# Optimization experiments

Hardware: AMD Instinct MI355X
Metric: run time of the kernel (lower is better)

The kernel has to match this reference:

```python
import jax, jax.numpy as jnp
import numpy as np

B, S, D, H = 8, 1024, 1024, 16
HD = D // H  # head dim = 64


def setup_inputs() -> dict:
    key = jax.random.key(0)
    ks = jax.random.split(key, 8)
    return {
        "hidden_states": jax.random.normal(ks[0], (B, S, D), dtype=jnp.float32),
        "attention_mask": jnp.zeros((B, 1, 1, S), dtype=jnp.float32),
        "Wq": jax.random.normal(ks[1], (D, D), dtype=jnp.float32) * (1.0 / np.sqrt(D)),
        "bq": jax.random.normal(ks[2], (D,), dtype=jnp.float32) * 0.02,
        "Wk": jax.random.normal(ks[3], (D, D), dtype=jnp.float32) * (1.0 / np.sqrt(D)),
        "bk": jax.random.normal(ks[4], (D,), dtype=jnp.float32) * 0.02,
        "Wv": jax.random.normal(ks[5], (D, D), dtype=jnp.float32) * (1.0 / np.sqrt(D)),
        "bv": jax.random.normal(ks[6], (D,), dtype=jnp.float32) * 0.02,
    }


def _split_heads(x):
    # [B,S,D] -> [B,H,S,HD]
    return x.reshape(B, S, H, HD).transpose(0, 2, 1, 3)


def reference(hidden_states, attention_mask, Wq, bq, Wk, bk, Wv, bv):
    q = _split_heads(hidden_states @ Wq + bq)
    k = _split_heads(hidden_states @ Wk + bk)
    v = _split_heads(hidden_states @ Wv + bv)
    # [B,H,S,S]
    scores = jnp.einsum("bhqd,bhkd->bhqk", q, k) / jnp.sqrt(jnp.float32(HD))
    scores = scores + attention_mask
    probs = jax.nn.softmax(scores, axis=-1)  # dropout p=0.0 (eval)
    ctx = jnp.einsum("bhqk,bhkd->bhqd", probs, v)
    # [B,H,S,HD] -> [B,S,D]
    return ctx.transpose(0, 2, 1, 3).reshape(B, S, D)
```

## Files before the change

kernel.cpp:

```cpp
#include <hip/hip_runtime.h>
#include <stdint.h>

#define BB 8
#define SS 1024
#define DD 1024
#define HH 16
#define HDIM 64

typedef __bf16 bf16x8 __attribute__((ext_vector_type(8)));
typedef float f32x4 __attribute__((ext_vector_type(4)));

__device__ __forceinline__ unsigned short f2bf(float f) {
    union { float f; unsigned u; } v; v.f = f;
    unsigned r = v.u + 0x7fff + ((v.u >> 16) & 1);
    return (unsigned short)(r >> 16);
}

__device__ __forceinline__ float exp2fast(float x) {
#if __has_builtin(__builtin_amdgcn_exp2f)
    return __builtin_amdgcn_exp2f(x);
#else
    return __expf(x * 0.69314718f);
#endif
}

__device__ __forceinline__ void async16(void* lds, const void* g) {
    __builtin_amdgcn_global_load_lds(
        (const __attribute__((address_space(1))) unsigned int*)g,
        (__attribute__((address_space(3))) unsigned int*)lds, 16, 0, 0);
}

__global__ __launch_bounds__(256) void convert_x(const float* __restrict__ x,
                                                 unsigned short* __restrict__ xb, int n) {
    int i = (blockIdx.x * 256 + threadIdx.x) * 4;
    if (i < n) {
        float4 f = *reinterpret_cast<const float4*>(x + i);
        ushort4 o;
        o.x = f2bf(f.x); o.y = f2bf(f.y); o.z = f2bf(f.z); o.w = f2bf(f.w);
        *reinterpret_cast<ushort4*>(xb + i) = o;
    }
}

__global__ __launch_bounds__(256) void transpose_w(const float* __restrict__ w0,
                                                   const float* __restrict__ w1,
                                                   const float* __restrict__ w2,
                                                   unsigned short* __restrict__ t0,
                                                   unsigned short* __restrict__ t1,
                                                   unsigned short* __restrict__ t2) {
    const float* w = (blockIdx.z == 0) ? w0 : (blockIdx.z == 1) ? w1 : w2;
    unsigned short* wt = (blockIdx.z == 0) ? t0 : (blockIdx.z == 1) ? t1 : t2;
    __shared__ unsigned short tile[64][65];
    int k0 = blockIdx.x * 64, n0 = blockIdx.y * 64;
    #pragma unroll
    for (int i = 0; i < 16; ++i) {
        int idx = threadIdx.x + i * 256;
        int r = idx >> 6, c = idx & 63;
        tile[r][c] = f2bf(w[(k0 + r) * DD + n0 + c]);
    }
    __syncthreads();
    #pragma unroll
    for (int i = 0; i < 16; ++i) {
        int idx = threadIdx.x + i * 256;
        int r = idx >> 6, c = idx & 63;
        wt[(n0 + r) * DD + k0 + c] = tile[c][r];
    }
}

__global__ __launch_bounds__(256) void gemm_qkv(
    const unsigned short* __restrict__ xb,
    const unsigned short* __restrict__ wt0, const unsigned short* __restrict__ wt1,
    const unsigned short* __restrict__ wt2,
    const float* __restrict__ b0, const float* __restrict__ b1, const float* __restrict__ b2,
    unsigned short* __restrict__ qo, unsigned short* __restrict__ ko,
    unsigned short* __restrict__ vto)
{
    const unsigned short* wt; const float* bias; unsigned short* out;
    if (blockIdx.z == 0)      { wt = wt0; bias = b0; out = qo; }
    else if (blockIdx.z == 1) { wt = wt1; bias = b1; out = ko; }
    else                      { wt = wt2; bias = b2; out = vto; }

    __shared__ unsigned short As[2][128 * 32];
    __shared__ unsigned short Bs[2][128 * 32];

    int m0 = blockIdx.x * 128, n0 = blockIdx.y * 128;
    int tid = threadIdx.x;
    int wave = tid >> 6, lane = tid & 63, lq = lane >> 4, lm = lane & 15;
    int wr = wave >> 1, wc = wave & 1;

    f32x4 acc[4][4] = {};

    int row0 = tid >> 2, s = tid & 3;
    int c0 = (s - (row0 >> 1)) & 3;
    const unsigned short* ga0 = xb + (m0 + row0) * DD + c0 * 8;
    const unsigned short* ga1 = ga0 + 64 * DD;
    const unsigned short* gb0 = wt + (n0 + row0) * DD + c0 * 8;
    const unsigned short* gb1 = gb0 + 64 * DD;

    int slot = ((lq + (lm >> 1)) & 3) * 8;

    async16(&As[0][tid * 8], ga0);  async16(&As[0][(tid + 256) * 8], ga1);
    async16(&Bs[0][tid * 8], gb0);  async16(&Bs[0][(tid + 256) * 8], gb1);
    ga0 += 32; ga1 += 32; gb0 += 32; gb1 += 32;

    for (int t = 0; t < 32; ++t) {
        int p = t & 1;
        __syncthreads();
        if (t < 31) {
            async16(&As[p ^ 1][tid * 8], ga0);  async16(&As[p ^ 1][(tid + 256) * 8], ga1);
            async16(&Bs[p ^ 1][tid * 8], gb0);  async16(&Bs[p ^ 1][(tid + 256) * 8], gb1);
            ga0 += 32; ga1 += 32; gb0 += 32; gb1 += 32;
        }
        bf16x8 a[4], b[4];
        #pragma unroll
        for (int i = 0; i < 4; ++i)
            a[i] = *reinterpret_cast<const bf16x8*>(&As[p][(wr * 64 + i * 16 + lm) * 32 + slot]);
        #pragma unroll
        for (int j = 0; j < 4; ++j)
            b[j] = *reinterpret_cast<const bf16x8*>(&Bs[p][(wc * 64 + j * 16 + lm) * 32 + slot]);
        #pragma unroll
        for (int i = 0; i < 4; ++i)
            #pragma unroll
            for (int j = 0; j < 4; ++j)
                acc[i][j] = __builtin_amdgcn_mfma_f32_16x16x32_bf16(a[i], b[j], acc[i][j], 0, 0, 0);
    }

    if (blockIdx.z == 2) {
        #pragma unroll
        for (int j = 0; j < 4; ++j) {
            int col = n0 + wc * 64 + j * 16 + lm;
            float bsv = bias[col];
            int h = col >> 6, hd = col & 63;
            #pragma unroll
            for (int i = 0; i < 4; ++i) {
                int m = m0 + wr * 64 + i * 16 + lq * 4;
                int b_ = m >> 10, sr = m & 1023;
                ushort4 pk;
                pk.x = f2bf(acc[i][j][0] + bsv);
                pk.y = f2bf(acc[i][j][1] + bsv);
                pk.z = f2bf(acc[i][j][2] + bsv);
                pk.w = f2bf(acc[i][j][3] + bsv);
                *reinterpret_cast<ushort4*>(out + (((b_ * HH + h) * HDIM + hd) << 10) + sr) = pk;
            }
        }
    } else {
        #pragma unroll
        for (int j = 0; j < 4; ++j) {
            int col = n0 + wc * 64 + j * 16 + lm;
            float bsv = bias[col];
            int h = col >> 6, hd = col & 63;
            #pragma unroll
            for (int i = 0; i < 4; ++i) {
                #pragma unroll
                for (int r = 0; r < 4; ++r) {
                    int m = m0 + wr * 64 + i * 16 + lq * 4 + r;
                    int b_ = m >> 10, sr = m & 1023;
                    out[(((b_ * HH + h) << 10) + sr) * HDIM + hd] = f2bf(acc[i][j][r] + bsv);
                }
            }
        }
    }
}

__global__ __launch_bounds__(256) void attention(
    const unsigned short* __restrict__ q,
    const unsigned short* __restrict__ k,
    const unsigned short* __restrict__ vt,
    const float* __restrict__ mask,
    float* __restrict__ out)
{
    __shared__ unsigned short Ks[2][64 * 64];
    __shared__ unsigned short Vs[2][64 * 64];
    __shared__ unsigned short Ps[4][16 * 72];
    __shared__ float msk[SS];

    int blk = blockIdx.x;
    int xcd = blk & 7, j = blk >> 3;
    int bh = (xcd << 4) + (j >> 4);
    int qt = j & 15;
    int b = bh >> 4, h = bh & 15;

    int tid = threadIdx.x;
    int wave = tid >> 6, lane = tid & 63, lq = lane >> 4, lm = lane & 15;

    const unsigned short* qp = q + (size_t)bh * SS * HDIM;
    const unsigned short* kp = k + (size_t)bh * SS * HDIM;
    const unsigned short* vp = vt + (size_t)bh * HDIM * SS;

    for (int i = tid; i < SS; i += 256) msk[i] = mask[b * SS + i] * 1.44269504f;

    int qrow = qt * 64 + wave * 16 + lm;
    bf16x8 qa0 = *reinterpret_cast<const bf16x8*>(qp + qrow * HDIM + lq * 8);
    bf16x8 qa1 = *reinterpret_cast<const bf16x8*>(qp + qrow * HDIM + 32 + lq * 8);

    float lsum = 0.f;
    f32x4 o[4] = {};

    int row0 = tid >> 3, sg = tid & 7;
    int cg = (sg - row0) & 7;
    const unsigned short* gk = kp + row0 * 64 + cg * 8;
    const unsigned short* gv = vp + row0 * SS + cg * 8;

    int sl0 = ((lq + lm) & 7) * 8;
    int sl1 = ((lq + lm + 4) & 7) * 8;

    async16(&Ks[0][tid * 8], gk);  async16(&Ks[0][(tid + 256) * 8], gk + 32 * 64);
    async16(&Vs[0][tid * 8], gv);  async16(&Vs[0][(tid + 256) * 8], gv + 32 * SS);
    gk += 64 * 64; gv += 64;

    unsigned short* Pw = Ps[wave];

    for (int t = 0; t < 16; ++t) {
        int p = t & 1;
        __syncthreads();
        if (t < 15) {
            async16(&Ks[p ^ 1][tid * 8], gk);  async16(&Ks[p ^ 1][(tid + 256) * 8], gk + 32 * 64);
            async16(&Vs[p ^ 1][tid * 8], gv);  async16(&Vs[p ^ 1][(tid + 256) * 8], gv + 32 * SS);
            gk += 64 * 64; gv += 64;
        }
        int kb0 = t * 64;

        f32x4 c[4];
        #pragma unroll
        for (int nb = 0; nb < 4; ++nb) {
            bf16x8 kf0 = *reinterpret_cast<const bf16x8*>(&Ks[p][(nb * 16 + lm) * 64 + sl0]);
            bf16x8 kf1 = *reinterpret_cast<const bf16x8*>(&Ks[p][(nb * 16 + lm) * 64 + sl1]);
            f32x4 z = {};
            z = __builtin_amdgcn_mfma_f32_16x16x32_bf16(kf0, qa0, z, 0, 0, 0);
            z = __builtin_amdgcn_mfma_f32_16x16x32_bf16(kf1, qa1, z, 0, 0, 0);
            c[nb] = z;
        }

        #pragma unroll
        for (int nb = 0; nb < 4; ++nb) {
            float4 mk = *reinterpret_cast<const float4*>(&msk[kb0 + nb * 16 + lq * 4]);
            unsigned u[4];
            #pragma unroll
            for (int r = 0; r < 4; ++r) {
                float e = exp2fast(fmaf(c[nb][r], 0.18033688f,
                                        reinterpret_cast<const float*>(&mk)[r]));
                union { float f; unsigned v; } cv; cv.f = e;
                u[r] = cv.v;
                union { unsigned v; float f; } tr; tr.v = cv.v & 0xffff0000u;
                lsum += tr.f;
            }
            uint2 pk;
            pk.x = __builtin_amdgcn_perm(u[1], u[0], 0x07060302u);
            pk.y = __builtin_amdgcn_perm(u[3], u[2], 0x07060302u);
            *reinterpret_cast<uint2*>(&Pw[lm * 72 + nb * 16 + lq * 4]) = pk;
        }

        #pragma unroll
        for (int ks = 0; ks < 2; ++ks) {
            bf16x8 pa = *reinterpret_cast<const bf16x8*>(&Pw[lm * 72 + ks * 32 + lq * 8]);
            int slv = (ks == 0) ? sl0 : sl1;
            #pragma unroll
            for (int nb2 = 0; nb2 < 4; ++nb2) {
                bf16x8 vf = *reinterpret_cast<const bf16x8*>(&Vs[p][(nb2 * 16 + lm) * 64 + slv]);
                o[nb2] = __builtin_amdgcn_mfma_f32_16x16x32_bf16(pa, vf, o[nb2], 0, 0, 0);
            }
        }
    }

    lsum += __shfl_xor(lsum, 16, 64);
    lsum += __shfl_xor(lsum, 32, 64);
    float linv[4];
    #pragma unroll
    for (int r = 0; r < 4; ++r)
        linv[r] = 1.0f / __shfl(lsum, lq * 4 + r, 64);

    #pragma unroll
    for (int nb2 = 0; nb2 < 4; ++nb2) {
        #pragma unroll
        for (int r = 0; r < 4; ++r) {
            int sr = qt * 64 + wave * 16 + lq * 4 + r;
            out[((size_t)(b * SS + sr)) * DD + h * HDIM + nb2 * 16 + lm] = o[nb2][r] * linv[r];
        }
    }
}

extern "C" void kernel_launch(void* const* d_in, const int* in_sizes, int n_in,
                              void* d_out, int out_size, void* d_ws, size_t ws_size,
                              hipStream_t stream) {
    const float* hs   = (const float*)d_in[0];
    const float* mask = (const float*)d_in[1];
    const float* Wq   = (const float*)d_in[2];
    const float* bq   = (const float*)d_in[3];
    const float* Wk   = (const float*)d_in[4];
    const float* bk   = (const float*)d_in[5];
    const float* Wv   = (const float*)d_in[6];
    const float* bv   = (const float*)d_in[7];
    float* out = (float*)d_out;

    char* ws = (char*)d_ws;
    unsigned short* Xb  = (unsigned short*)(ws);
    unsigned short* WT0 = (unsigned short*)(ws + 16777216);
    unsigned short* WT1 = (unsigned short*)(ws + 18874368);
    unsigned short* WT2 = (unsigned short*)(ws + 20971520);
    unsigned short* qw  = (unsigned short*)(ws + 23068672);
    unsigned short* kw  = (unsigned short*)(ws + 39845888);
    unsigned short* vtw = (unsigned short*)(ws + 56623104);

    convert_x<<<8192, 256, 0, stream>>>(hs, Xb, BB * SS * DD);
    transpose_w<<<dim3(16, 16, 3), 256, 0, stream>>>(Wq, Wk, Wv, WT0, WT1, WT2);
    gemm_qkv<<<dim3(64, 8, 3), 256, 0, stream>>>(Xb, WT0, WT1, WT2,
                                                 bq, bk, bv, qw, kw, vtw);
    attention<<<2048, 256, 0, stream>>>(qw, kw, vtw, mask, out);
}
```

Measured before the change: 249.3 us.

## Fuse prep kernels, remap GEMM blocks per XCD, stream A from registers, interleave attention

Merges the activation conversion and weight transpose into one launch. The QKV GEMM now uses a 1D grid that groups tiles sharing a weight strip onto the same XCD, and loads the A operand straight from global memory into double-buffered registers instead of LDS. The GEMM epilogue switches to a cheaper round-half-up bf16 pack. In attention, the mask is read from global memory instead of being staged in LDS. The QK^T, softmax and PV steps are split into halves and interleaved so MFMA work can overlap exp work, and the P buffer uses a swizzled 64-wide layout. These changes trade the round-to-nearest-even rounding for a slightly different rounding and add register pressure in the GEMM.

Result: slower. 280.8 us (+12.6%).

```diff
diff --git a/kernel.cpp b/kernel.cpp
--- a/kernel.cpp
+++ b/kernel.cpp
@@ -14,6 +14,11 @@
     union { float f; unsigned u; } v; v.f = f;
     unsigned r = v.u + 0x7fff + ((v.u >> 16) & 1);
     return (unsigned short)(r >> 16);
+}
+
+__device__ __forceinline__ unsigned pk2bf(float f0, float f1) {
+    union { float f; unsigned u; } a, b; a.f = f0; b.f = f1;
+    return __builtin_amdgcn_perm(b.u + 0x8000u, a.u + 0x8000u, 0x07060302u);
 }
 
 __device__ __forceinline__ float exp2fast(float x) {
@@ -30,38 +35,39 @@
         (__attribute__((address_space(3))) unsigned int*)lds, 16, 0, 0);
 }
 
-__global__ __launch_bounds__(256) void convert_x(const float* __restrict__ x,
-                                                 unsigned short* __restrict__ xb, int n) {
-    int i = (blockIdx.x * 256 + threadIdx.x) * 4;
-    if (i < n) {
+__global__ __launch_bounds__(256) void prep(
+    const float* __restrict__ x, unsigned short* __restrict__ xb,
+    const float* __restrict__ w0, const float* __restrict__ w1,
+    const float* __restrict__ w2,
+    unsigned short* __restrict__ t0, unsigned short* __restrict__ t1,
+    unsigned short* __restrict__ t2)
+{
+    __shared__ unsigned short tile[64][65];
+    int bid = blockIdx.x;
+    if (bid < 8192) {
+        int i = (bid * 256 + threadIdx.x) * 4;
         float4 f = *reinterpret_cast<const float4*>(x + i);
         ushort4 o;
         o.x = f2bf(f.x); o.y = f2bf(f.y); o.z = f2bf(f.z); o.w = f2bf(f.w);
         *reinterpret_cast<ushort4*>(xb + i) = o;
-    }
-}
-
-__global__ __launch_bounds__(256) void transpose_w(const float* __restrict__ w0,
-                                                   const float* __restrict__ w1,
-                                                   const float* __restrict__ w2,
-                                                   unsigned short* __restrict__ t0,
-                                                   unsigned short* __restrict__ t1,
-                                                   unsigned short* __restrict__ t2) {
-    const float* w = (blockIdx.z == 0) ? w0 : (blockIdx.z == 1) ? w1 : w2;
-    unsigned short* wt = (blockIdx.z == 0) ? t0 : (blockIdx.z == 1) ? t1 : t2;
-    __shared__ unsigned short tile[64][65];
-    int k0 = blockIdx.x * 64, n0 = blockIdx.y * 64;
+        return;
+    }
+    int idx = bid - 8192;
+    int z = idx >> 8, rem = idx & 255;
+    const float* w = (z == 0) ? w0 : (z == 1) ? w1 : w2;
+    unsigned short* wt = (z == 0) ? t0 : (z == 1) ? t1 : t2;
+    int k0 = (rem & 15) * 64, n0 = (rem >> 4) * 64;
     #pragma unroll
     for (int i = 0; i < 16; ++i) {
-        int idx = threadIdx.x + i * 256;
-        int r = idx >> 6, c = idx & 63;
+        int id = threadIdx.x + i * 256;
+        int r = id >> 6, c = id & 63;
         tile[r][c] = f2bf(w[(k0 + r) * DD + n0 + c]);
     }
     __syncthreads();
     #pragma unroll
     for (int i = 0; i < 16; ++i) {
-        int idx = threadIdx.x + i * 256;
-        int r = idx >> 6, c = idx & 63;
+        int id = threadIdx.x + i * 256;
+        int r = id >> 6, c = id & 63;
         wt[(n0 + r) * DD + k0 + c] = tile[c][r];
     }
 }
@@ -74,46 +80,55 @@
     unsigned short* __restrict__ qo, unsigned short* __restrict__ ko,
     unsigned short* __restrict__ vto)
 {
+    int bid = blockIdx.x;
+    int xcd = bid & 7, g = bid >> 3;
+    int strip = xcd * 3 + (g % 3);
+    int mt = g / 3;
+    int nt = strip & 7, z = strip >> 3;
+
     const unsigned short* wt; const float* bias; unsigned short* out;
-    if (blockIdx.z == 0)      { wt = wt0; bias = b0; out = qo; }
-    else if (blockIdx.z == 1) { wt = wt1; bias = b1; out = ko; }
-    else                      { wt = wt2; bias = b2; out = vto; }
-
-    __shared__ unsigned short As[2][128 * 32];
+    if (z == 0)      { wt = wt0; bias = b0; out = qo; }
+    else if (z == 1) { wt = wt1; bias = b1; out = ko; }
+    else             { wt = wt2; bias = b2; out = vto; }
+
     __shared__ unsigned short Bs[2][128 * 32];
 
-    int m0 = blockIdx.x * 128, n0 = blockIdx.y * 128;
+    int m0 = mt * 128, n0 = nt * 128;
     int tid = threadIdx.x;
     int wave = tid >> 6, lane = tid & 63, lq = lane >> 4, lm = lane & 15;
     int wr = wave >> 1, wc = wave & 1;
 
     f32x4 acc[4][4] = {};
 
-    int row0 = tid >> 2, s = tid & 3;
-    int c0 = (s - (row0 >> 1)) & 3;
-    const unsigned short* ga0 = xb + (m0 + row0) * DD + c0 * 8;
-    const unsigned short* ga1 = ga0 + 64 * DD;
+    int row0 = tid >> 2, s4 = tid & 3;
+    int c0 = (s4 - (row0 >> 1)) & 3;
     const unsigned short* gb0 = wt + (n0 + row0) * DD + c0 * 8;
     const unsigned short* gb1 = gb0 + 64 * DD;
 
+    const unsigned short* aBase = xb + (m0 + wr * 64 + lm) * DD + lq * 8;
+
     int slot = ((lq + (lm >> 1)) & 3) * 8;
 
-    async16(&As[0][tid * 8], ga0);  async16(&As[0][(tid + 256) * 8], ga1);
-    async16(&Bs[0][tid * 8], gb0);  async16(&Bs[0][(tid + 256) * 8], gb1);
-    ga0 += 32; ga1 += 32; gb0 += 32; gb1 += 32;
-
+    bf16x8 a[2][4];
+
+    async16(&Bs[0][tid * 8], gb0);
+    async16(&Bs[0][(tid + 256) * 8], gb1);
+    #pragma unroll
+    for (int i = 0; i < 4; ++i)
+        a[0][i] = *reinterpret_cast<const bf16x8*>(aBase + i * 16 * DD);
+
+    #pragma unroll
     for (int t = 0; t < 32; ++t) {
         int p = t & 1;
         __syncthreads();
         if (t < 31) {
-            async16(&As[p ^ 1][tid * 8], ga0);  async16(&As[p ^ 1][(tid + 256) * 8], ga1);
-            async16(&Bs[p ^ 1][tid * 8], gb0);  async16(&Bs[p ^ 1][(tid + 256) * 8], gb1);
-            ga0 += 32; ga1 += 32; gb0 += 32; gb1 += 32;
-        }
-        bf16x8 a[4], b[4];
-        #pragma unroll
-        for (int i = 0; i < 4; ++i)
-            a[i] = *reinterpret_cast<const bf16x8*>(&As[p][(wr * 64 + i * 16 + lm) * 32 + slot]);
+            async16(&Bs[p ^ 1][tid * 8], gb0 + (t + 1) * 32);
+            async16(&Bs[p ^ 1][(tid + 256) * 8], gb1 + (t + 1) * 32);
+            #pragma unroll
+            for (int i = 0; i < 4; ++i)
+                a[p ^ 1][i] = *reinterpret_cast<const bf16x8*>(aBase + i * 16 * DD + (t + 1) * 32);
+        }
+        bf16x8 b[4];
         #pragma unroll
         for (int j = 0; j < 4; ++j)
             b[j] = *reinterpret_cast<const bf16x8*>(&Bs[p][(wc * 64 + j * 16 + lm) * 32 + slot]);
@@ -121,10 +136,10 @@
         for (int i = 0; i < 4; ++i)
             #pragma unroll
             for (int j = 0; j < 4; ++j)
-                acc[i][j] = __builtin_amdgcn_mfma_f32_16x16x32_bf16(a[i], b[j], acc[i][j], 0, 0, 0);
-    }
-
-    if (blockIdx.z == 2) {
+                acc[i][j] = __builtin_amdgcn_mfma_f32_16x16x32_bf16(a[p][i], b[j], acc[i][j], 0, 0, 0);
+    }
+
+    if (z == 2) {
         #pragma unroll
         for (int j = 0; j < 4; ++j) {
             int col = n0 + wc * 64 + j * 16 + lm;
@@ -134,12 +149,10 @@
             for (int i = 0; i < 4; ++i) {
                 int m = m0 + wr * 64 + i * 16 + lq * 4;
                 int b_ = m >> 10, sr = m & 1023;
-                ushort4 pk;
-                pk.x = f2bf(acc[i][j][0] + bsv);
-                pk.y = f2bf(acc[i][j][1] + bsv);
-                pk.z = f2bf(acc[i][j][2] + bsv);
-                pk.w = f2bf(acc[i][j][3] + bsv);
-                *reinterpret_cast<ushort4*>(out + (((b_ * HH + h) * HDIM + hd) << 10) + sr) = pk;
+                uint2 pk;
+                pk.x = pk2bf(acc[i][j][0] + bsv, acc[i][j][1] + bsv);
+                pk.y = pk2bf(acc[i][j][2] + bsv, acc[i][j][3] + bsv);
+                *reinterpret_cast<uint2*>(out + (((b_ * HH + h) * HDIM + hd) << 10) + sr) = pk;
             }
         }
     } else {
@@ -154,7 +167,9 @@
                 for (int r = 0; r < 4; ++r) {
                     int m = m0 + wr * 64 + i * 16 + lq * 4 + r;
                     int b_ = m >> 10, sr = m & 1023;
-                    out[(((b_ * HH + h) << 10) + sr) * HDIM + hd] = f2bf(acc[i][j][r] + bsv);
+                    union { float f; unsigned u; } cv; cv.f = acc[i][j][r] + bsv;
+                    out[(((b_ * HH + h) << 10) + sr) * HDIM + hd] =
+                        (unsigned short)((cv.u + 0x8000u) >> 16);
                 }
             }
         }
@@ -170,8 +185,7 @@
 {
     __shared__ unsigned short Ks[2][64 * 64];
     __shared__ unsigned short Vs[2][64 * 64];
-    __shared__ unsigned short Ps[4][16 * 72];
-    __shared__ float msk[SS];
+    __shared__ unsigned short Ps[4][16 * 64];
 
     int blk = blockIdx.x;
     int xcd = blk & 7, j = blk >> 3;
@@ -185,8 +199,7 @@
     const unsigned short* qp = q + (size_t)bh * SS * HDIM;
     const unsigned short* kp = k + (size_t)bh * SS * HDIM;
     const unsigned short* vp = vt + (size_t)bh * HDIM * SS;
-
-    for (int i = tid; i < SS; i += 256) msk[i] = mask[b * SS + i] * 1.44269504f;
+    const float* maskb = mask + b * SS;
 
     int qrow = qt * 64 + wave * 16 + lm;
     bf16x8 qa0 = *reinterpret_cast<const bf16x8*>(qp + qrow * HDIM + lq * 8);
@@ -202,12 +215,14 @@
 
     int sl0 = ((lq + lm) & 7) * 8;
     int sl1 = ((lq + lm + 4) & 7) * 8;
+    unsigned short* Pw = Ps[wave];
+    int pwbase = lm * 64 + (lq & 1) * 4;
+    int prd0 = lm * 64 + sl0;
+    int prd1 = lm * 64 + sl1;
 
     async16(&Ks[0][tid * 8], gk);  async16(&Ks[0][(tid + 256) * 8], gk + 32 * 64);
     async16(&Vs[0][tid * 8], gv);  async16(&Vs[0][(tid + 256) * 8], gv + 32 * SS);
     gk += 64 * 64; gv += 64;
-
-    unsigned short* Pw = Ps[wave];
 
     for (int t = 0; t < 16; ++t) {
         int p = t & 1;
@@ -219,43 +234,79 @@
         }
         int kb0 = t * 64;
 
+        float4 mk[4];
+        #pragma unroll
+        for (int nb = 0; nb < 4; ++nb)
+            mk[nb] = *reinterpret_cast<const float4*>(maskb + kb0 + nb * 16 + lq * 4);
+
         f32x4 c[4];
         #pragma unroll
-        for (int nb = 0; nb < 4; ++nb) {
+        for (int nb = 0; nb < 2; ++nb) {
             bf16x8 kf0 = *reinterpret_cast<const bf16x8*>(&Ks[p][(nb * 16 + lm) * 64 + sl0]);
             bf16x8 kf1 = *reinterpret_cast<const bf16x8*>(&Ks[p][(nb * 16 + lm) * 64 + sl1]);
-            f32x4 z = {};
-            z = __builtin_amdgcn_mfma_f32_16x16x32_bf16(kf0, qa0, z, 0, 0, 0);
-            z = __builtin_amdgcn_mfma_f32_16x16x32_bf16(kf1, qa1, z, 0, 0, 0);
-            c[nb] = z;
-        }
-
-        #pragma unroll
-        for (int nb = 0; nb < 4; ++nb) {
-            float4 mk = *reinterpret_cast<const float4*>(&msk[kb0 + nb * 16 + lq * 4]);
+            f32x4 zz = {};
+            zz = __builtin_amdgcn_mfma_f32_16x16x32_bf16(kf0, qa0, zz, 0, 0, 0);
+            zz = __builtin_amdgcn_mfma_f32_16x16x32_bf16(kf1, qa1, zz, 0, 0, 0);
+            c[nb] = zz;
+        }
+        #pragma unroll
+        for (int nb = 0; nb < 2; ++nb) {
             unsigned u[4];
             #pragma unroll
             for (int r = 0; r < 4; ++r) {
                 float e = exp2fast(fmaf(c[nb][r], 0.18033688f,
-                                        reinterpret_cast<const float*>(&mk)[r]));
+                                        reinterpret_cast<const float*>(&mk[nb])[r] * 1.44269504f));
                 union { float f; unsigned v; } cv; cv.f = e;
-                u[r] = cv.v;
-                union { unsigned v; float f; } tr; tr.v = cv.v & 0xffff0000u;
+                u[r] = cv.v + 0x8000u;
+                union { unsigned v; float f; } tr; tr.v = u[r] & 0xffff0000u;
                 lsum += tr.f;
             }
             uint2 pk;
             pk.x = __builtin_amdgcn_perm(u[1], u[0], 0x07060302u);
             pk.y = __builtin_amdgcn_perm(u[3], u[2], 0x07060302u);
-            *reinterpret_cast<uint2*>(&Pw[lm * 72 + nb * 16 + lq * 4]) = pk;
-        }
-
-        #pragma unroll
-        for (int ks = 0; ks < 2; ++ks) {
-            bf16x8 pa = *reinterpret_cast<const bf16x8*>(&Pw[lm * 72 + ks * 32 + lq * 8]);
-            int slv = (ks == 0) ? sl0 : sl1;
+            *reinterpret_cast<uint2*>(
+                &Pw[pwbase + (((nb * 2 + (lq >> 1)) + lm) & 7) * 8]) = pk;
+        }
+        #pragma unroll
+        for (int nb = 2; nb < 4; ++nb) {
+            bf16x8 kf0 = *reinterpret_cast<const bf16x8*>(&Ks[p][(nb * 16 + lm) * 64 + sl0]);
+            bf16x8 kf1 = *reinterpret_cast<const bf16x8*>(&Ks[p][(nb * 16 + lm) * 64 + sl1]);
+            f32x4 zz = {};
+            zz = __builtin_amdgcn_mfma_f32_16x16x32_bf16(kf0, qa0, zz, 0, 0, 0);
+            zz = __builtin_amdgcn_mfma_f32_16x16x32_bf16(kf1, qa1, zz, 0, 0, 0);
+            c[nb] = zz;
+        }
+        {
+            bf16x8 pa = *reinterpret_cast<const bf16x8*>(&Pw[prd0]);
             #pragma unroll
             for (int nb2 = 0; nb2 < 4; ++nb2) {
-                bf16x8 vf = *reinterpret_cast<const bf16x8*>(&Vs[p][(nb2 * 16 + lm) * 64 + slv]);
+                bf16x8 vf = *reinterpret_cast<const bf16x8*>(&Vs[p][(nb2 * 16 + lm) * 64 + sl0]);
+                o[nb2] = __builtin_amdgcn_mfma_f32_16x16x32_bf16(pa, vf, o[nb2], 0, 0, 0);
+            }
+        }
+        #pragma unroll
+        for (int nb = 2; nb < 4; ++nb) {
+            unsigned u[4];
+            #pragma unroll
+            for (int r = 0; r < 4; ++r) {
+                float e = exp2fast(fmaf(c[nb][r], 0.18033688f,
+                                        reinterpret_cast<const float*>(&mk[nb])[r] * 1.44269504f));
+                union { float f; unsigned v; } cv; cv.f = e;
+                u[r] = cv.v + 0x8000u;
+                union { unsigned v; float f; } tr; tr.v = u[r] & 0xffff0000u;
+                lsum += tr.f;
+            }
+            uint2 pk;
+            pk.x = __builtin_amdgcn_perm(u[1], u[0], 0x07060302u);
+            pk.y = __builtin_amdgcn_perm(u[3], u[2], 0x07060302u);
+            *reinterpret_cast<uint2*>(
+                &Pw[pwbase + (((nb * 2 + (lq >> 1)) + lm) & 7) * 8]) = pk;
+        }
+        {
+            bf16x8 pa = *reinterpret_cast<const bf16x8*>(&Pw[prd1]);
+            #pragma unroll
+            for (int nb2 = 0; nb2 < 4; ++nb2) {
+                bf16x8 vf = *reinterpret_cast<const bf16x8*>(&Vs[p][(nb2 * 16 + lm) * 64 + sl1]);
                 o[nb2] = __builtin_amdgcn_mfma_f32_16x16x32_bf16(pa, vf, o[nb2], 0, 0, 0);
             }
         }
@@ -300,9 +351,8 @@
     unsigned short* kw  = (unsigned short*)(ws + 39845888);
     unsigned short* vtw = (unsigned short*)(ws + 56623104);
 
-    convert_x<<<8192, 256, 0, stream>>>(hs, Xb, BB * SS * DD);
-    transpose_w<<<dim3(16, 16, 3), 256, 0, stream>>>(Wq, Wk, Wv, WT0, WT1, WT2);
-    gemm_qkv<<<dim3(64, 8, 3), 256, 0, stream>>>(Xb, WT0, WT1, WT2,
-                                                 bq, bk, bv, qw, kw, vtw);
+    prep<<<8960, 256, 0, stream>>>(hs, Xb, Wq, Wk, Wv, WT0, WT1, WT2);
+    gemm_qkv<<<1536, 256, 0, stream>>>(Xb, WT0, WT1, WT2,
+                                       bq, bk, bv, qw, kw, vtw);
     attention<<<2048, 256, 0, stream>>>(qw, kw, vtw, mask, out);
 }
```
